# Kernel tuning notes

Hardware: AMD Instinct MI355X
Metric: run time of the kernel (lower is better)

Reference implementation:

```python
import jax, jax.numpy as jnp
import numpy as np

B, S, IN, H, OUT, L = 64, 2048, 208, 100, 98, 2


def setup_inputs() -> dict:
    key = jax.random.key(0)
    ks = jax.random.split(key, 11)
    sc = 1.0 / np.sqrt(H)  # pytorch GRU init scale
    return {
        "sequence": jax.random.normal(ks[0], (B, S, IN), jnp.float32),
        "h0": jnp.zeros((L, B, H), jnp.float32),
        "w_ih_l0": jax.random.normal(ks[1], (3 * H, IN), jnp.float32) * sc,
        "w_hh_l0": jax.random.normal(ks[2], (3 * H, H), jnp.float32) * sc,
        "b_ih_l0": jax.random.normal(ks[3], (3 * H,), jnp.float32) * sc,
        "b_hh_l0": jax.random.normal(ks[4], (3 * H,), jnp.float32) * sc,
        "w_ih_l1": jax.random.normal(ks[5], (3 * H, H), jnp.float32) * sc,
        "w_hh_l1": jax.random.normal(ks[6], (3 * H, H), jnp.float32) * sc,
        "b_ih_l1": jax.random.normal(ks[7], (3 * H,), jnp.float32) * sc,
        "b_hh_l1": jax.random.normal(ks[8], (3 * H,), jnp.float32) * sc,
        "w_out": jax.random.normal(ks[9], (OUT, H), jnp.float32) * sc,
        "b_out": jax.random.normal(ks[10], (OUT,), jnp.float32) * sc,
    }


def _gru_layer(x, h0, w_ih, w_hh, b_ih, b_hh):
    # x: (B,S,Din), h0: (B,H). PyTorch GRU gate order: r, z, n.
    Hd = h0.shape[-1]
    xg = jnp.einsum("bsi,gi->bsg", x, w_ih) + b_ih  # (B,S,3H) input projections, batched GEMM

    def step(h, xg_t):
        hg = h @ w_hh.T + b_hh  # (B,3H)
        xr, xz, xn = xg_t[:, :Hd], xg_t[:, Hd:2 * Hd], xg_t[:, 2 * Hd:]
        hr, hz, hn = hg[:, :Hd], hg[:, Hd:2 * Hd], hg[:, 2 * Hd:]
        r = jax.nn.sigmoid(xr + hr)
        z = jax.nn.sigmoid(xz + hz)
        n = jnp.tanh(xn + r * hn)
        h_new = (1.0 - z) * n + z * h
        return h_new, h_new

    h_last, ys = jax.lax.scan(step, h0, jnp.swapaxes(xg, 0, 1))  # scan over time
    return jnp.swapaxes(ys, 0, 1), h_last  # (B,S,H)


def reference(sequence, h0, w_ih_l0, w_hh_l0, b_ih_l0, b_hh_l0,
              w_ih_l1, w_hh_l1, b_ih_l1, b_hh_l1, w_out, b_out):
    # 2-layer unidirectional GRU (eval mode: inter-layer dropout inactive) + linear head
    y0, _ = _gru_layer(sequence, h0[0], w_ih_l0, w_hh_l0, b_ih_l0, b_hh_l0)
    y1, _ = _gru_layer(y0, h0[1], w_ih_l1, w_hh_l1, b_ih_l1, b_hh_l1)
    return jnp.einsum("bsh,oh->bso", y1, w_out) + b_out  # (B,S,OUT)
```

## Files before the change

kernel.cpp:

```cpp
#include <hip/hip_runtime.h>


#define GB_BM 64
#define GB_BN 64
#define GB_BK 16

__global__ __launch_bounds__(256)
void gemm_bias(const float* __restrict__ A, const float* __restrict__ W,
               const float* __restrict__ bias, float* __restrict__ C,
               int Sc, long a_bs, long a_ss, long c_bs, long c_ss,
               int N, int K)
{
    __shared__ float As[GB_BK][68];
    __shared__ float Bs[GB_BK][68];
    const int tid = threadIdx.x;
    const int m0 = blockIdx.x * GB_BM;
    const int n0 = blockIdx.y * GB_BN;

    const int lm = tid >> 2;
    const int lk = (tid & 3) << 2;
    const int row = m0 + lm;
    const float* arow = A + (long)(row / Sc) * a_bs + (long)(row % Sc) * a_ss;
    const int wrow = n0 + lm;
    const float* wrp = W + (long)wrow * K;
    const bool wv_ok = (wrow < N);

    const int tx = tid & 15;
    const int ty = tid >> 4;

    float acc[4][4] = {};

    for (int k0 = 0; k0 < K; k0 += GB_BK) {
        float4 av, bv;
        if (k0 + GB_BK <= K) {
            av = *(const float4*)(arow + k0 + lk);
            bv = wv_ok ? *(const float4*)(wrp + k0 + lk) : make_float4(0.f,0.f,0.f,0.f);
        } else {
            av = make_float4(0.f,0.f,0.f,0.f);
            bv = make_float4(0.f,0.f,0.f,0.f);
            const int kb = k0 + lk;
            if (kb + 0 < K) { av.x = arow[kb+0]; if (wv_ok) bv.x = wrp[kb+0]; }
            if (kb + 1 < K) { av.y = arow[kb+1]; if (wv_ok) bv.y = wrp[kb+1]; }
            if (kb + 2 < K) { av.z = arow[kb+2]; if (wv_ok) bv.z = wrp[kb+2]; }
            if (kb + 3 < K) { av.w = arow[kb+3]; if (wv_ok) bv.w = wrp[kb+3]; }
        }
        As[lk+0][lm] = av.x; As[lk+1][lm] = av.y; As[lk+2][lm] = av.z; As[lk+3][lm] = av.w;
        Bs[lk+0][lm] = bv.x; Bs[lk+1][lm] = bv.y; Bs[lk+2][lm] = bv.z; Bs[lk+3][lm] = bv.w;
        __syncthreads();
        #pragma unroll
        for (int kk = 0; kk < GB_BK; kk++) {
            float4 a  = *(const float4*)&As[kk][ty << 2];
            float4 bb = *(const float4*)&Bs[kk][tx << 2];
            float ar[4] = {a.x, a.y, a.z, a.w};
            float br[4] = {bb.x, bb.y, bb.z, bb.w};
            #pragma unroll
            for (int i = 0; i < 4; i++)
                #pragma unroll
                for (int j = 0; j < 4; j++)
                    acc[i][j] += ar[i] * br[j];
        }
        __syncthreads();
    }

    #pragma unroll
    for (int i = 0; i < 4; i++) {
        const int r = m0 + (ty << 2) + i;
        float* crow = C + (long)(r / Sc) * c_bs + (long)(r % Sc) * c_ss;
        #pragma unroll
        for (int j = 0; j < 4; j++) {
            const int col = n0 + (tx << 2) + j;
            if (col < N) crow[col] = acc[i][j] + bias[col];
        }
    }
}


#define RING_W 256
#define KPUB   16

__device__ __forceinline__ float fsig(float x)  { return 1.f / (1.f + __expf(-x)); }
__device__ __forceinline__ float ftanh(float x) { return 1.f - 2.f / (1.f + __expf(2.f * x)); }

__device__ __forceinline__ void bar_lgkm() {
    asm volatile("s_waitcnt lgkmcnt(0)" ::: "memory");
    __builtin_amdgcn_sched_barrier(0);
    __builtin_amdgcn_s_barrier();
}
__device__ __forceinline__ void bar_full() {
    asm volatile("s_waitcnt vmcnt(0) lgkmcnt(0)" ::: "memory");
    __builtin_amdgcn_sched_barrier(0);
    __builtin_amdgcn_s_barrier();
}
__device__ __forceinline__ void wait_ge(int* p, int tgt) {
    int spins = 0;
    while (__hip_atomic_load(p, __ATOMIC_ACQUIRE, __HIP_MEMORY_SCOPE_AGENT) < tgt) {
        __builtin_amdgcn_s_sleep(2);
        if (++spins > (1 << 22)) break;
    }
}

__global__ __launch_bounds__(640, 3)
void gru_fused(const float* __restrict__ xg0,
               const float* __restrict__ w_hh0, const float* __restrict__ b_hh0,
               const float* __restrict__ w_ih1, const float* __restrict__ b_ih1,
               const float* __restrict__ w_hh1, const float* __restrict__ b_hh1,
               const float* __restrict__ w_out, const float* __restrict__ b_out,
               const float* __restrict__ h_init,
               float* __restrict__ ring,
               int* prog0, int* cons1,
               float* __restrict__ out,
               int S)
{
    __shared__ __align__(16) float hs[2][104];

    const int tid   = threadIdx.x;
    const int layer = blockIdx.x >> 6;
    const int b     = blockIdx.x & 63;

    const int lane  = tid & 63;
    const int wid   = tid >> 6;
    const int pair  = lane >> 1;
    const int jl    = pair / 3;
    const int role  = pair - 3 * jl;
    const int halfd = tid & 1;
    const int j     = wid * 10 + jl;
    const bool d1   = (lane < 60);
    const bool evenl= d1 && (halfd == 0);
    const bool gate = evenl && (role == 0);
    const bool loadA= evenl && (role <= 1);
    const int jc    = (j < 100) ? j : 99;
    const int row1  = role * 100 + jc;

    const int g2    = tid >> 1;
    const int n2    = layer ? 98 : 300;
    const bool act2 = (g2 < n2);
    const int g2c   = act2 ? g2 : 0;

    int* myprog = prog0 + b * 32;
    int* mycons = cons1 + b * 32;

    const float* w_hh = layer ? w_hh1 : w_hh0;
    const float* W2   = layer ? w_out : w_ih1;

    float4 wv[13], wv2[13];
    {
        const float* p = w_hh + row1 * 100 + halfd * 48;
        #pragma unroll
        for (int i = 0; i < 13; i++) wv[i] = *(const float4*)(p + 4 * i);
        if (!halfd) wv[12] = make_float4(0.f, 0.f, 0.f, 0.f);
        const float* q = W2 + g2c * 100 + halfd * 48;
        #pragma unroll
        for (int i = 0; i < 13; i++) wv2[i] = *(const float4*)(q + 4 * i);
        if (!halfd) wv2[12] = make_float4(0.f, 0.f, 0.f, 0.f);
    }
    const float bhh   = (layer ? b_hh1 : b_hh0)[row1];
    const float bias2 = (layer ? b_out : b_ih1)[g2c];

    float hcur = 0.f;
    if (gate) hcur = h_init[layer * 6400 + b * 100 + j];
    if (tid < 100) hs[0][tid] = h_init[layer * 6400 + b * 100 + tid];

    float* ringb      = ring + (size_t)b * RING_W * 300;
    const float* xgb  = xg0 + (size_t)b * (size_t)S * 300;
    float* outb       = out + (size_t)b * (size_t)S * 98;

    float xA_n = 0.f, xN_n = 0.f;

    if (layer == 0) {
        if (loadA) xA_n = xgb[row1];
        if (gate)  xN_n = xgb[200 + j];
    } else {
        if (tid == 0) wait_ge(myprog, (S < KPUB + 1) ? S : (KPUB + 1));
    }
    __syncthreads();
    if (layer == 1) {
        if (loadA) xA_n = ringb[row1];
        if (gate)  xN_n = ringb[200 + j];
    }

    for (int t = 0; t < S; t++) {
        const int cur = t & 1;
        const int nxt = cur ^ 1;
        const float xA = xA_n, xN = xN_n;

        if (t + 1 < S) {
            const float* src = (layer == 0)
                ? xgb + (size_t)(t + 1) * 300
                : ringb + (size_t)((t + 1) & (RING_W - 1)) * 300;
            if (loadA) xA_n = src[row1];
            if (gate)  xN_n = src[200 + j];
        }

        const float4* h4p = (const float4*)hs[cur];
        const int base = halfd * 12;
        float a0 = 0.f, a1 = 0.f, a2 = 0.f, a3 = 0.f;
        #pragma unroll
        for (int i = 0; i < 13; i++) {
            const float4 h4 = h4p[base + i];
            const float4 w = wv[i];
            a0 += w.x * h4.x; a1 += w.y * h4.y;
            a2 += w.z * h4.z; a3 += w.w * h4.w;
        }
        float tot = (a0 + a2) + (a1 + a3);
        tot += __shfl_down(tot, 1);
        float val = tot + bhh;
        if (loadA) val += xA;
        const float zpre = __shfl(val, lane + 2);
        const float hnv  = __shfl(val, lane + 4);

        if (gate) {
            const float r = fsig(val);
            const float z = fsig(zpre);
            const float n = ftanh(xN + r * hnv);
            hcur = (1.f - z) * n + z * hcur;
            hs[nxt][j] = hcur;
        }

        if (act2 && t > 0) {
            float c0 = 0.f, c1 = 0.f, c2 = 0.f, c3 = 0.f;
            #pragma unroll
            for (int i = 0; i < 13; i++) {
                const float4 h4 = h4p[base + i];
                const float4 w = wv2[i];
                c0 += w.x * h4.x; c1 += w.y * h4.y;
                c2 += w.z * h4.z; c3 += w.w * h4.w;
            }
            float tot2 = (c0 + c2) + (c1 + c3);
            tot2 += __shfl_down(tot2, 1);
            if (!halfd) {
                if (layer == 0)
                    ringb[(size_t)((t - 1) & (RING_W - 1)) * 300 + g2] = tot2 + bias2;
                else
                    outb[(size_t)(t - 1) * 98 + g2] = tot2 + bias2;
            }
        }

        if (((t + 1) & (KPUB - 1)) == 0) {
            if (layer == 0) {
                bar_full();
                if (tid == 0) {
                    __hip_atomic_store(myprog, t, __ATOMIC_RELEASE, __HIP_MEMORY_SCOPE_AGENT);
                    const int need = t - 240;
                    if (need > 0) wait_ge(mycons, need);
                }
            } else {
                if (tid == 0) {
                    __hip_atomic_store(mycons, t, __ATOMIC_RELEASE, __HIP_MEMORY_SCOPE_AGENT);
                    int tgt = t + 2 + KPUB;
                    if (tgt > S) tgt = S;
                    wait_ge(myprog, tgt);
                }
                bar_lgkm();
            }
        } else {
            bar_lgkm();
        }
    }

    {
        const float4* h4p = (const float4*)hs[S & 1];
        const int base = halfd * 12;
        if (act2) {
            float c0 = 0.f, c1 = 0.f, c2 = 0.f, c3 = 0.f;
            #pragma unroll
            for (int i = 0; i < 13; i++) {
                const float4 h4 = h4p[base + i];
                const float4 w = wv2[i];
                c0 += w.x * h4.x; c1 += w.y * h4.y;
                c2 += w.z * h4.z; c3 += w.w * h4.w;
            }
            float tot2 = (c0 + c2) + (c1 + c3);
            tot2 += __shfl_down(tot2, 1);
            if (!halfd) {
                if (layer == 0)
                    ringb[(size_t)((S - 1) & (RING_W - 1)) * 300 + g2] = tot2 + bias2;
                else
                    outb[(size_t)(S - 1) * 98 + g2] = tot2 + bias2;
            }
        }
    }
    if (layer == 0) {
        bar_full();
        if (tid == 0)
            __hip_atomic_store(myprog, S, __ATOMIC_RELEASE, __HIP_MEMORY_SCOPE_AGENT);
    }
}


extern "C" void kernel_launch(void* const* d_in, const int* in_sizes, int n_in,
                              void* d_out, int out_size, void* d_ws, size_t ws_size,
                              hipStream_t stream)
{
    const float* seq    = (const float*)d_in[0];
    const float* h0     = (const float*)d_in[1];
    const float* w_ih0  = (const float*)d_in[2];
    const float* w_hh0  = (const float*)d_in[3];
    const float* b_ih0  = (const float*)d_in[4];
    const float* b_hh0  = (const float*)d_in[5];
    const float* w_ih1  = (const float*)d_in[6];
    const float* w_hh1  = (const float*)d_in[7];
    const float* b_ih1  = (const float*)d_in[8];
    const float* b_hh1  = (const float*)d_in[9];
    const float* w_out  = (const float*)d_in[10];
    const float* b_out  = (const float*)d_in[11];
    float* out = (float*)d_out;

    const int B = 64, S = 2048, IN = 208, G = 300;

    int* prog0 = (int*)d_ws;
    int* cons1 = prog0 + 64 * 32;
    float* xg0 = (float*)(cons1 + 64 * 32);
    float* ringbuf = xg0 + (size_t)B * S * G;

    hipMemsetAsync(d_ws, 0, 2 * 64 * 32 * sizeof(int), stream);

    const dim3 blk(256);
    const dim3 gX((B * S) / GB_BM, (G + GB_BN - 1) / GB_BN);
    gemm_bias<<<gX, blk, 0, stream>>>(seq, w_ih0, b_ih0, xg0,
                                      S, (long)S * IN, (long)IN,
                                      (long)S * G, (long)G, G, IN);

    gru_fused<<<dim3(128), dim3(640), 0, stream>>>(
        xg0, w_hh0, b_hh0, w_ih1, b_ih1, w_hh1, b_hh1, w_out, b_out,
        h0, ringbuf, prog0, cons1, out, S);
}
```

Measured before the change: 2.948 ms.

## Halve GRU block size, give each lane four weight rows, use DPP reduction

Recurrent blocks drop from 640 to 320 threads (5 waves). Each lane pair now holds four register-resident weight rows: two recurrent gate rows and two rows of the next-stage projection. The r and z gates are computed directly in the gate lane, and the n-gate partial sums are fetched with one cross-lane shuffle. The two-lane partial-sum reduction uses a DPP quad swap instead of shfl_down. The aim is to cut the per-step barrier cost and wave count on the serial critical path, at the price of four times the FMA work per lane and much higher register pressure.

```diff
diff --git a/kernel.cpp b/kernel.cpp
--- a/kernel.cpp
+++ b/kernel.cpp
@@ -98,8 +98,12 @@
         if (++spins > (1 << 22)) break;
     }
 }
-
-__global__ __launch_bounds__(640, 3)
+__device__ __forceinline__ float dpp_swap1(float x) {
+    int r = __builtin_amdgcn_update_dpp(0, __float_as_int(x), 0xB1, 0xF, 0xF, false);
+    return __int_as_float(r);
+}
+
+__global__ __launch_bounds__(320, 2)
 void gru_fused(const float* __restrict__ xg0,
                const float* __restrict__ w_hh0, const float* __restrict__ b_hh0,
                const float* __restrict__ w_ih1, const float* __restrict__ b_ih1,
@@ -117,121 +121,136 @@
     const int layer = blockIdx.x >> 6;
     const int b     = blockIdx.x & 63;
 
+    const int wv    = tid >> 6;
     const int lane  = tid & 63;
-    const int wid   = tid >> 6;
-    const int pair  = lane >> 1;
-    const int jl    = pair / 3;
-    const int role  = pair - 3 * jl;
-    const int halfd = tid & 1;
-    const int j     = wid * 10 + jl;
-    const bool d1   = (lane < 60);
-    const bool evenl= d1 && (halfd == 0);
-    const bool gate = evenl && (role == 0);
-    const bool loadA= evenl && (role <= 1);
-    const int jc    = (j < 100) ? j : 99;
-    const int row1  = role * 100 + jc;
-
-    const int g2    = tid >> 1;
-    const int n2    = layer ? 98 : 300;
-    const bool act2 = (g2 < n2);
-    const int g2c   = act2 ? g2 : 0;
+    const int p     = lane >> 1;
+    const int halfd = lane & 1;
+    const int jw    = 20 * wv;
+    const int pj    = (p < 20) ? p : 19;
+    const int j     = jw + pj;
+    const bool gate = (halfd == 0) && (p < 20);
+
+    int rA1, rB1;
+    if (p < 20)      { rA1 = jw + p;              rB1 = 100 + jw + p; }
+    else if (p < 30) { rA1 = 200 + jw + 2*(p-20); rB1 = rA1 + 1; }
+    else             { rA1 = 0;                   rB1 = 1; }
+
+    const int e   = wv * 32 + p;
+    const int N2  = layer ? 98 : 300;
+    const bool actA2 = (e < N2);
+    const bool actB2 = (e + 160 < N2);
+    const int r2A = actA2 ? e : 0;
+    const int r2B = actB2 ? e + 160 : 0;
 
     int* myprog = prog0 + b * 32;
     int* mycons = cons1 + b * 32;
 
     const float* w_hh = layer ? w_hh1 : w_hh0;
     const float* W2   = layer ? w_out : w_ih1;
-
-    float4 wv[13], wv2[13];
+    const float* bhh  = layer ? b_hh1 : b_hh0;
+    const float* b2   = layer ? b_out : b_ih1;
+
+    float4 wA1[13], wB1[13], wA2[13], wB2[13];
     {
-        const float* p = w_hh + row1 * 100 + halfd * 48;
-        #pragma unroll
-        for (int i = 0; i < 13; i++) wv[i] = *(const float4*)(p + 4 * i);
-        if (!halfd) wv[12] = make_float4(0.f, 0.f, 0.f, 0.f);
-        const float* q = W2 + g2c * 100 + halfd * 48;
-        #pragma unroll
-        for (int i = 0; i < 13; i++) wv2[i] = *(const float4*)(q + 4 * i);
-        if (!halfd) wv2[12] = make_float4(0.f, 0.f, 0.f, 0.f);
-    }
-    const float bhh   = (layer ? b_hh1 : b_hh0)[row1];
-    const float bias2 = (layer ? b_out : b_ih1)[g2c];
+        const float* pa = w_hh + rA1 * 100 + halfd * 48;
+        const float* pb = w_hh + rB1 * 100 + halfd * 48;
+        const float* qa = W2   + r2A * 100 + halfd * 48;
+        const float* qb = W2   + r2B * 100 + halfd * 48;
+        #pragma unroll
+        for (int i = 0; i < 13; i++) {
+            wA1[i] = *(const float4*)(pa + 4 * i);
+            wB1[i] = *(const float4*)(pb + 4 * i);
+            wA2[i] = *(const float4*)(qa + 4 * i);
+            wB2[i] = *(const float4*)(qb + 4 * i);
+        }
+        if (!halfd) {
+            wA1[12] = make_float4(0.f,0.f,0.f,0.f);
+            wB1[12] = make_float4(0.f,0.f,0.f,0.f);
+            wA2[12] = make_float4(0.f,0.f,0.f,0.f);
+            wB2[12] = make_float4(0.f,0.f,0.f,0.f);
+        }
+    }
+    const float bR = bhh[j], bZ = bhh[100 + j], bN = bhh[200 + j];
+    const float b2A = b2[r2A], b2B = b2[r2B];
 
     float hcur = 0.f;
     if (gate) hcur = h_init[layer * 6400 + b * 100 + j];
     if (tid < 100) hs[0][tid] = h_init[layer * 6400 + b * 100 + tid];
 
-    float* ringb      = ring + (size_t)b * RING_W * 300;
-    const float* xgb  = xg0 + (size_t)b * (size_t)S * 300;
-    float* outb       = out + (size_t)b * (size_t)S * 98;
-
-    float xA_n = 0.f, xN_n = 0.f;
+    float* ringb     = ring + (size_t)b * RING_W * 300;
+    const float* xgb = xg0 + (size_t)b * (size_t)S * 300;
+    float* outb      = out + (size_t)b * (size_t)S * 98;
+
+    float xRn = 0.f, xZn = 0.f, xNn = 0.f;
 
     if (layer == 0) {
-        if (loadA) xA_n = xgb[row1];
-        if (gate)  xN_n = xgb[200 + j];
+        if (gate) {
+            xRn = xgb[j]; xZn = xgb[100 + j]; xNn = xgb[200 + j];
+        }
     } else {
         if (tid == 0) wait_ge(myprog, (S < KPUB + 1) ? S : (KPUB + 1));
     }
     __syncthreads();
-    if (layer == 1) {
-        if (loadA) xA_n = ringb[row1];
-        if (gate)  xN_n = ringb[200 + j];
-    }
+    if (layer == 1 && gate) {
+        xRn = ringb[j]; xZn = ringb[100 + j]; xNn = ringb[200 + j];
+    }
+
+    const int slb = 40 + (pj & ~1);
 
     for (int t = 0; t < S; t++) {
         const int cur = t & 1;
         const int nxt = cur ^ 1;
-        const float xA = xA_n, xN = xN_n;
-
-        if (t + 1 < S) {
+        const float xR = xRn, xZ = xZn, xN = xNn;
+
+        if (gate && t + 1 < S) {
             const float* src = (layer == 0)
                 ? xgb + (size_t)(t + 1) * 300
                 : ringb + (size_t)((t + 1) & (RING_W - 1)) * 300;
-            if (loadA) xA_n = src[row1];
-            if (gate)  xN_n = src[200 + j];
+            xRn = src[j]; xZn = src[100 + j]; xNn = src[200 + j];
         }
 
         const float4* h4p = (const float4*)hs[cur];
         const int base = halfd * 12;
-        float a0 = 0.f, a1 = 0.f, a2 = 0.f, a3 = 0.f;
+        float a0[4] = {0.f,0.f,0.f,0.f}, a1[4] = {0.f,0.f,0.f,0.f};
+        float a2[4] = {0.f,0.f,0.f,0.f}, a3[4] = {0.f,0.f,0.f,0.f};
         #pragma unroll
         for (int i = 0; i < 13; i++) {
             const float4 h4 = h4p[base + i];
-            const float4 w = wv[i];
-            a0 += w.x * h4.x; a1 += w.y * h4.y;
-            a2 += w.z * h4.z; a3 += w.w * h4.w;
-        }
-        float tot = (a0 + a2) + (a1 + a3);
-        tot += __shfl_down(tot, 1);
-        float val = tot + bhh;
-        if (loadA) val += xA;
-        const float zpre = __shfl(val, lane + 2);
-        const float hnv  = __shfl(val, lane + 4);
+            a0[0] += wA1[i].x * h4.x; a1[0] += wA1[i].y * h4.y;
+            a2[0] += wA1[i].z * h4.z; a3[0] += wA1[i].w * h4.w;
+            a0[1] += wB1[i].x * h4.x; a1[1] += wB1[i].y * h4.y;
+            a2[1] += wB1[i].z * h4.z; a3[1] += wB1[i].w * h4.w;
+            a0[2] += wA2[i].x * h4.x; a1[2] += wA2[i].y * h4.y;
+            a2[2] += wA2[i].z * h4.z; a3[2] += wA2[i].w * h4.w;
+            a0[3] += wB2[i].x * h4.x; a1[3] += wB2[i].y * h4.y;
+            a2[3] += wB2[i].z * h4.z; a3[3] += wB2[i].w * h4.w;
+        }
+        float full[4];
+        #pragma unroll
+        for (int g = 0; g < 4; g++) {
+            const float s = (a0[g] + a2[g]) + (a1[g] + a3[g]);
+            full[g] = s + dpp_swap1(s);
+        }
+
+        const float nA = __shfl(full[0], slb);
+        const float nB = __shfl(full[1], slb);
 
         if (gate) {
-            const float r = fsig(val);
-            const float z = fsig(zpre);
-            const float n = ftanh(xN + r * hnv);
+            const float dN = (pj & 1) ? nB : nA;
+            const float r = fsig(xR + full[0] + bR);
+            const float z = fsig(xZ + full[1] + bZ);
+            const float n = ftanh(xN + r * (dN + bN));
             hcur = (1.f - z) * n + z * hcur;
             hs[nxt][j] = hcur;
         }
 
-        if (act2 && t > 0) {
-            float c0 = 0.f, c1 = 0.f, c2 = 0.f, c3 = 0.f;
-            #pragma unroll
-            for (int i = 0; i < 13; i++) {
-                const float4 h4 = h4p[base + i];
-                const float4 w = wv2[i];
-                c0 += w.x * h4.x; c1 += w.y * h4.y;
-                c2 += w.z * h4.z; c3 += w.w * h4.w;
-            }
-            float tot2 = (c0 + c2) + (c1 + c3);
-            tot2 += __shfl_down(tot2, 1);
-            if (!halfd) {
-                if (layer == 0)
-                    ringb[(size_t)((t - 1) & (RING_W - 1)) * 300 + g2] = tot2 + bias2;
-                else
-                    outb[(size_t)(t - 1) * 98 + g2] = tot2 + bias2;
+        if (t > 0 && halfd == 0) {
+            if (layer == 0) {
+                float* dst = ringb + (size_t)((t - 1) & (RING_W - 1)) * 300;
+                if (actA2) dst[r2A] = full[2] + b2A;
+                if (actB2) dst[r2B] = full[3] + b2B;
+            } else {
+                if (actA2) outb[(size_t)(t - 1) * 98 + r2A] = full[2] + b2A;
             }
         }
 
@@ -260,22 +279,25 @@
     {
         const float4* h4p = (const float4*)hs[S & 1];
         const int base = halfd * 12;
-        if (act2) {
-            float c0 = 0.f, c1 = 0.f, c2 = 0.f, c3 = 0.f;
-            #pragma unroll
-            for (int i = 0; i < 13; i++) {
-                const float4 h4 = h4p[base + i];
-                const float4 w = wv2[i];
-                c0 += w.x * h4.x; c1 += w.y * h4.y;
-                c2 += w.z * h4.z; c3 += w.w * h4.w;
-            }
-            float tot2 = (c0 + c2) + (c1 + c3);
-            tot2 += __shfl_down(tot2, 1);
-            if (!halfd) {
-                if (layer == 0)
-                    ringb[(size_t)((S - 1) & (RING_W - 1)) * 300 + g2] = tot2 + bias2;
-                else
-                    outb[(size_t)(S - 1) * 98 + g2] = tot2 + bias2;
+        float c0A = 0.f, c1A = 0.f, c2A = 0.f, c3A = 0.f;
+        float c0B = 0.f, c1B = 0.f, c2B = 0.f, c3B = 0.f;
+        #pragma unroll
+        for (int i = 0; i < 13; i++) {
+            const float4 h4 = h4p[base + i];
+            c0A += wA2[i].x * h4.x; c1A += wA2[i].y * h4.y;
+            c2A += wA2[i].z * h4.z; c3A += wA2[i].w * h4.w;
+            c0B += wB2[i].x * h4.x; c1B += wB2[i].y * h4.y;
+            c2B += wB2[i].z * h4.z; c3B += wB2[i].w * h4.w;
+        }
+        float sA = (c0A + c2A) + (c1A + c3A); sA += dpp_swap1(sA);
+        float sB = (c0B + c2B) + (c1B + c3B); sB += dpp_swap1(sB);
+        if (halfd == 0) {
+            if (layer == 0) {
+                float* dst = ringb + (size_t)((S - 1) & (RING_W - 1)) * 300;
+                if (actA2) dst[r2A] = sA + b2A;
+                if (actB2) dst[r2B] = sB + b2B;
+            } else {
+                if (actA2) outb[(size_t)(S - 1) * 98 + r2A] = sA + b2A;
             }
         }
     }
@@ -320,7 +342,7 @@
                                       S, (long)S * IN, (long)IN,
                                       (long)S * G, (long)G, G, IN);
 
-    gru_fused<<<dim3(128), dim3(640), 0, stream>>>(
+    gru_fused<<<dim3(128), dim3(320), 0, stream>>>(
         xg0, w_hh0, b_hh0, w_ih1, b_ih1, w_hh1, b_hh1, w_out, b_out,
         h0, ringbuf, prog0, cons1, out, S);
 }
```

After: 3.594 ms. +21.9%, slower.
